# Kernel optimization log

Measured on AMD Instinct MI355X. Metric: run time of the kernel, lower is better.

The kernel has to match this reference:

```python
import jax, jax.numpy as jnp
import numpy as np

B_SZ, T, I, H = 32, 2048, 128, 256

def setup_inputs() -> dict:
    key = jax.random.key(0)
    k1, k2, k3, k4 = jax.random.split(key, 4)
    x = jax.random.normal(k1, (B_SZ, T, I), dtype=jnp.float32)
    A = jax.random.normal(k2, (H, H), dtype=jnp.float32) * 0.01
    Bm = jax.random.normal(k3, (I, H), dtype=jnp.float32) * 0.01
    C = jax.random.normal(k4, (H, H), dtype=jnp.float32) * 0.01
    return {"x": x, "A": A, "Bm": Bm, "C": C}

def reference(x, A, Bm, C):
    # Precompute input projection for all timesteps: [B, T, H]
    xB = jnp.einsum('bti,ih->bth', x, Bm)
    h0 = jnp.zeros((x.shape[0], A.shape[0]), dtype=x.dtype)

    def step(h, xb_t):
        h = jnp.tanh(h @ A + xb_t)  # [B, H]
        return h, h

    # scan over time: xB transposed to [T, B, H]
    _, hs = jax.lax.scan(step, h0, jnp.swapaxes(xB, 0, 1))
    # outputs: h_t @ C at every step -> [B, T, H]
    out = jnp.einsum('tbh,hk->btk', hs, C)
    return out
```

## Files before the change

### kernel.cpp

```cpp
#include <hip/hip_runtime.h>
#include <math.h>

#define B_SZ 32
#define T_LEN 2048
#define I_DIM 128
#define H_DIM 256
#define ROWS 32

__global__ __launch_bounds__(256) void xb_proj(const float* __restrict__ x,
                                               const float* __restrict__ Bm,
                                               float* __restrict__ xB) {
    __shared__ float4 xt[ROWS][I_DIM / 4 + 1];
    const int tid = threadIdx.x;
    const int j = tid;
    const long r0 = (long)blockIdx.x * ROWS;

    const float4* xg = (const float4*)(x + r0 * I_DIM);
#pragma unroll
    for (int i = 0; i < 4; ++i) {
        int f = tid + i * 256;
        int rr = f >> 5;
        int kg = f & 31;
        xt[rr][kg] = xg[rr * 32 + kg];
    }
    __syncthreads();

    float acc[ROWS];
#pragma unroll
    for (int r = 0; r < ROWS; ++r) acc[r] = 0.f;

    for (int k = 0; k < I_DIM; k += 4) {
        float w0 = Bm[(k + 0) * H_DIM + j];
        float w1 = Bm[(k + 1) * H_DIM + j];
        float w2 = Bm[(k + 2) * H_DIM + j];
        float w3 = Bm[(k + 3) * H_DIM + j];
#pragma unroll
        for (int r = 0; r < ROWS; ++r) {
            float4 hv = xt[r][k >> 2];
            acc[r] = fmaf(hv.x, w0, acc[r]);
            acc[r] = fmaf(hv.y, w1, acc[r]);
            acc[r] = fmaf(hv.z, w2, acc[r]);
            acc[r] = fmaf(hv.w, w3, acc[r]);
        }
    }
#pragma unroll
    for (int r = 0; r < ROWS; ++r)
        xB[(r0 + r) * H_DIM + j] = acc[r];
}

__global__ __launch_bounds__(512, 2) void rnn_scan(const float* __restrict__ A,
                                                   const float* __restrict__ xB,
                                                   float* __restrict__ hs) {
    __shared__ __align__(16) float h[H_DIM];
    __shared__ float red[H_DIM];
    const int tid = threadIdx.x;
    const int j = tid & 255;
    const int kh = tid >> 8;
    const int b = blockIdx.x;

    float Areg[128];
#pragma unroll
    for (int kk = 0; kk < 128; ++kk)
        Areg[kk] = A[(kh * 128 + kk) * H_DIM + j];

    if (tid < H_DIM) h[tid] = 0.f;

    const float* xbp = xB + (long)b * T_LEN * H_DIM + j;
    float* hp = hs + (long)b * T_LEN * H_DIM + j;
    float xb_next = xbp[0];

    __syncthreads();

    for (int t = 0; t < T_LEN; ++t) {
        float p0 = 0.f, p1 = 0.f, p2 = 0.f, p3 = 0.f;
        const float4* h4 = (const float4*)&h[kh * 128];
#pragma unroll
        for (int kk = 0; kk < 128; kk += 4) {
            float4 hv = h4[kk >> 2];
            p0 = fmaf(hv.x, Areg[kk + 0], p0);
            p1 = fmaf(hv.y, Areg[kk + 1], p1);
            p2 = fmaf(hv.z, Areg[kk + 2], p2);
            p3 = fmaf(hv.w, Areg[kk + 3], p3);
        }
        float partial = (p0 + p1) + (p2 + p3);
        if (kh == 0) red[j] = partial;
        __syncthreads();
        if (kh == 1) {
            float y = partial + red[j] + xb_next;
            float hn = tanhf(y);
            h[j] = hn;
            hp[(long)t * H_DIM] = hn;
            if (t + 1 < T_LEN) xb_next = xbp[(long)(t + 1) * H_DIM];
        }
        __syncthreads();
    }
}

__global__ __launch_bounds__(256) void out_proj(float* __restrict__ hs_out,
                                                const float* __restrict__ C) {
    __shared__ float4 ht[ROWS][H_DIM / 4 + 1];
    const int tid = threadIdx.x;
    const int j = tid;
    const long r0 = (long)blockIdx.x * ROWS;

    const float4* hg = (const float4*)(hs_out + r0 * H_DIM);
#pragma unroll
    for (int i = 0; i < 8; ++i) {
        int f = tid + i * 256;
        int rr = f >> 6;
        int kg = f & 63;
        ht[rr][kg] = hg[rr * 64 + kg];
    }
    __syncthreads();

    float acc[ROWS];
#pragma unroll
    for (int r = 0; r < ROWS; ++r) acc[r] = 0.f;

    for (int k = 0; k < H_DIM; k += 4) {
        float w0 = C[(k + 0) * H_DIM + j];
        float w1 = C[(k + 1) * H_DIM + j];
        float w2 = C[(k + 2) * H_DIM + j];
        float w3 = C[(k + 3) * H_DIM + j];
#pragma unroll
        for (int r = 0; r < ROWS; ++r) {
            float4 hv = ht[r][k >> 2];
            acc[r] = fmaf(hv.x, w0, acc[r]);
            acc[r] = fmaf(hv.y, w1, acc[r]);
            acc[r] = fmaf(hv.z, w2, acc[r]);
            acc[r] = fmaf(hv.w, w3, acc[r]);
        }
    }
#pragma unroll
    for (int r = 0; r < ROWS; ++r)
        hs_out[(r0 + r) * H_DIM + j] = acc[r];
}

extern "C" void kernel_launch(void* const* d_in, const int* in_sizes, int n_in,
                              void* d_out, int out_size, void* d_ws, size_t ws_size,
                              hipStream_t stream) {
    const float* x  = (const float*)d_in[0];
    const float* A  = (const float*)d_in[1];
    const float* Bm = (const float*)d_in[2];
    const float* C  = (const float*)d_in[3];
    float* out = (float*)d_out;
    float* xB  = (float*)d_ws;

    const int R = B_SZ * T_LEN;

    xb_proj<<<R / ROWS, 256, 0, stream>>>(x, Bm, xB);
    rnn_scan<<<B_SZ, 512, 0, stream>>>(A, xB, out);
    out_proj<<<R / ROWS, 256, 0, stream>>>(out, C);
}
```

Before: 1.969 ms.

## Hold full A column in registers, read h from global, drop LDS staging

```diff
diff --git a/kernel.cpp b/kernel.cpp
--- a/kernel.cpp
+++ b/kernel.cpp
@@ -7,40 +7,39 @@
 #define H_DIM 256
 #define ROWS 32
 
+#define REP64(M) M(0)M(1)M(2)M(3)M(4)M(5)M(6)M(7)M(8)M(9)M(10)M(11)M(12)M(13)M(14)M(15) \
+                 M(16)M(17)M(18)M(19)M(20)M(21)M(22)M(23)M(24)M(25)M(26)M(27)M(28)M(29)M(30)M(31) \
+                 M(32)M(33)M(34)M(35)M(36)M(37)M(38)M(39)M(40)M(41)M(42)M(43)M(44)M(45)M(46)M(47) \
+                 M(48)M(49)M(50)M(51)M(52)M(53)M(54)M(55)M(56)M(57)M(58)M(59)M(60)M(61)M(62)M(63)
+
+__device__ __forceinline__ float fast_tanh(float y) {
+    float e = __expf(2.f * y);
+    return 1.f - 2.f / (e + 1.f);
+}
+
 __global__ __launch_bounds__(256) void xb_proj(const float* __restrict__ x,
                                                const float* __restrict__ Bm,
                                                float* __restrict__ xB) {
-    __shared__ float4 xt[ROWS][I_DIM / 4 + 1];
-    const int tid = threadIdx.x;
-    const int j = tid;
+    const int j = threadIdx.x;
     const long r0 = (long)blockIdx.x * ROWS;
-
-    const float4* xg = (const float4*)(x + r0 * I_DIM);
-#pragma unroll
-    for (int i = 0; i < 4; ++i) {
-        int f = tid + i * 256;
-        int rr = f >> 5;
-        int kg = f & 31;
-        xt[rr][kg] = xg[rr * 32 + kg];
-    }
-    __syncthreads();
 
     float acc[ROWS];
 #pragma unroll
     for (int r = 0; r < ROWS; ++r) acc[r] = 0.f;
 
-    for (int k = 0; k < I_DIM; k += 4) {
-        float w0 = Bm[(k + 0) * H_DIM + j];
-        float w1 = Bm[(k + 1) * H_DIM + j];
-        float w2 = Bm[(k + 2) * H_DIM + j];
-        float w3 = Bm[(k + 3) * H_DIM + j];
+#pragma unroll 4
+    for (int k4 = 0; k4 < I_DIM / 4; ++k4) {
+        const float wx = Bm[(4 * k4 + 0) * H_DIM + j];
+        const float wy = Bm[(4 * k4 + 1) * H_DIM + j];
+        const float wz = Bm[(4 * k4 + 2) * H_DIM + j];
+        const float ww = Bm[(4 * k4 + 3) * H_DIM + j];
 #pragma unroll
         for (int r = 0; r < ROWS; ++r) {
-            float4 hv = xt[r][k >> 2];
-            acc[r] = fmaf(hv.x, w0, acc[r]);
-            acc[r] = fmaf(hv.y, w1, acc[r]);
-            acc[r] = fmaf(hv.z, w2, acc[r]);
-            acc[r] = fmaf(hv.w, w3, acc[r]);
+            float4 xv = *(const float4*)(x + (r0 + r) * I_DIM + 4 * k4);
+            acc[r] = fmaf(xv.x, wx, acc[r]);
+            acc[r] = fmaf(xv.y, wy, acc[r]);
+            acc[r] = fmaf(xv.z, wz, acc[r]);
+            acc[r] = fmaf(xv.w, ww, acc[r]);
         }
     }
 #pragma unroll
@@ -48,87 +47,73 @@
         xB[(r0 + r) * H_DIM + j] = acc[r];
 }
 
-__global__ __launch_bounds__(512, 2) void rnn_scan(const float* __restrict__ A,
+__global__ __launch_bounds__(256, 1) void rnn_scan(const float* __restrict__ A,
                                                    const float* __restrict__ xB,
                                                    float* __restrict__ hs) {
-    __shared__ __align__(16) float h[H_DIM];
-    __shared__ float red[H_DIM];
-    const int tid = threadIdx.x;
-    const int j = tid & 255;
-    const int kh = tid >> 8;
+    const int j = threadIdx.x;
     const int b = blockIdx.x;
 
-    float Areg[128];
-#pragma unroll
-    for (int kk = 0; kk < 128; ++kk)
-        Areg[kk] = A[(kh * 128 + kk) * H_DIM + j];
+#define ADECL(K) float4 a##K;
+    REP64(ADECL)
+#undef ADECL
+#define ALOAD(K) a##K = make_float4(A[(4 * K + 0) * H_DIM + j], \
+                                    A[(4 * K + 1) * H_DIM + j], \
+                                    A[(4 * K + 2) * H_DIM + j], \
+                                    A[(4 * K + 3) * H_DIM + j]);
+    REP64(ALOAD)
+#undef ALOAD
 
-    if (tid < H_DIM) h[tid] = 0.f;
+    const long base = (long)b * T_LEN * H_DIM;
+    const float* __restrict__ xbp = xB + base + j;
+    float* __restrict__ hp = hs + base + j;
 
-    const float* xbp = xB + (long)b * T_LEN * H_DIM + j;
-    float* hp = hs + (long)b * T_LEN * H_DIM + j;
-    float xb_next = xbp[0];
-
+    float xbn = xbp[0];
+    float hn = fast_tanh(xbn);
+    hp[0] = hn;
+    xbn = xbp[H_DIM];
     __syncthreads();
 
-    for (int t = 0; t < T_LEN; ++t) {
-        float p0 = 0.f, p1 = 0.f, p2 = 0.f, p3 = 0.f;
-        const float4* h4 = (const float4*)&h[kh * 128];
-#pragma unroll
-        for (int kk = 0; kk < 128; kk += 4) {
-            float4 hv = h4[kk >> 2];
-            p0 = fmaf(hv.x, Areg[kk + 0], p0);
-            p1 = fmaf(hv.y, Areg[kk + 1], p1);
-            p2 = fmaf(hv.z, Areg[kk + 2], p2);
-            p3 = fmaf(hv.w, Areg[kk + 3], p3);
-        }
-        float partial = (p0 + p1) + (p2 + p3);
-        if (kh == 0) red[j] = partial;
-        __syncthreads();
-        if (kh == 1) {
-            float y = partial + red[j] + xb_next;
-            float hn = tanhf(y);
-            h[j] = hn;
-            hp[(long)t * H_DIM] = hn;
-            if (t + 1 < T_LEN) xb_next = xbp[(long)(t + 1) * H_DIM];
-        }
+    for (int t = 1; t < T_LEN; ++t) {
+        const float4* __restrict__ h4 =
+            (const float4*)(hs + base + (long)(t - 1) * H_DIM);
+        float y0 = 0.f, y1 = 0.f, y2 = 0.f, y3 = 0.f;
+#define FMA4(K) { float4 hv = h4[K]; \
+        y0 = fmaf(hv.x, a##K.x, y0); \
+        y1 = fmaf(hv.y, a##K.y, y1); \
+        y2 = fmaf(hv.z, a##K.z, y2); \
+        y3 = fmaf(hv.w, a##K.w, y3); }
+        REP64(FMA4)
+#undef FMA4
+        float y = (y0 + y1) + (y2 + y3) + xbn;
+        hn = fast_tanh(y);
+        hp[(long)t * H_DIM] = hn;
+        if (t + 1 < T_LEN) xbn = xbp[(long)(t + 1) * H_DIM];
         __syncthreads();
     }
 }
 
 __global__ __launch_bounds__(256) void out_proj(float* __restrict__ hs_out,
                                                 const float* __restrict__ C) {
-    __shared__ float4 ht[ROWS][H_DIM / 4 + 1];
-    const int tid = threadIdx.x;
-    const int j = tid;
+    const int j = threadIdx.x;
     const long r0 = (long)blockIdx.x * ROWS;
-
-    const float4* hg = (const float4*)(hs_out + r0 * H_DIM);
-#pragma unroll
-    for (int i = 0; i < 8; ++i) {
-        int f = tid + i * 256;
-        int rr = f >> 6;
-        int kg = f & 63;
-        ht[rr][kg] = hg[rr * 64 + kg];
-    }
-    __syncthreads();
 
     float acc[ROWS];
 #pragma unroll
     for (int r = 0; r < ROWS; ++r) acc[r] = 0.f;
 
-    for (int k = 0; k < H_DIM; k += 4) {
-        float w0 = C[(k + 0) * H_DIM + j];
-        float w1 = C[(k + 1) * H_DIM + j];
-        float w2 = C[(k + 2) * H_DIM + j];
-        float w3 = C[(k + 3) * H_DIM + j];
+#pragma unroll 4
+    for (int k4 = 0; k4 < H_DIM / 4; ++k4) {
+        const float wx = C[(4 * k4 + 0) * H_DIM + j];
+        const float wy = C[(4 * k4 + 1) * H_DIM + j];
+        const float wz = C[(4 * k4 + 2) * H_DIM + j];
+        const float ww = C[(4 * k4 + 3) * H_DIM + j];
 #pragma unroll
         for (int r = 0; r < ROWS; ++r) {
-            float4 hv = ht[r][k >> 2];
-            acc[r] = fmaf(hv.x, w0, acc[r]);
-            acc[r] = fmaf(hv.y, w1, acc[r]);
-            acc[r] = fmaf(hv.z, w2, acc[r]);
-            acc[r] = fmaf(hv.w, w3, acc[r]);
+            float4 hv = *(const float4*)(hs_out + (r0 + r) * H_DIM + 4 * k4);
+            acc[r] = fmaf(hv.x, wx, acc[r]);
+            acc[r] = fmaf(hv.y, wy, acc[r]);
+            acc[r] = fmaf(hv.z, wz, acc[r]);
+            acc[r] = fmaf(hv.w, ww, acc[r]);
         }
     }
 #pragma unroll
@@ -149,6 +134,6 @@
     const int R = B_SZ * T_LEN;
 
     xb_proj<<<R / ROWS, 256, 0, stream>>>(x, Bm, xB);
-    rnn_scan<<<B_SZ, 512, 0, stream>>>(A, xB, out);
+    rnn_scan<<<B_SZ, 256, 0, stream>>>(A, xB, out);
     out_proj<<<R / ROWS, 256, 0, stream>>>(out, C);
 }
```

Result: slower. 4.823 ms (+144.9%).
